# Kernel optimization log

Hardware: AMD Instinct MI355X
Metric: run time of the kernel (lower is better)

Reference implementation:

```python
import jax, jax.numpy as jnp
import numpy as np


def _entropy(x):
    # x: [..., C]; rowwise entropy of softmax(x) along last axis
    logp = jax.nn.log_softmax(x, axis=-1)
    return -(jnp.exp(logp) * logp).sum(-1)


def setup_inputs() -> dict:
    key = jax.random.key(0)
    C, E = 8192, 512
    prototypes = jax.random.normal(key, (C, E), dtype=jnp.float32)
    return {"prototypes": prototypes}


def reference(prototypes):
    C, E = prototypes.shape
    # F.normalize(p=2, dim=1): divide by L2 norm clamped to 1e-12
    norm = jnp.sqrt(jnp.sum(prototypes * prototypes, axis=1, keepdims=True))
    p = prototypes / jnp.maximum(norm, 1e-12)
    # Gram matrix [C, C] (fused matmul instead of broadcast-mul-sum)
    proto_logits = jnp.einsum("ce,de->cd", p, p)
    proto_logits_sum = proto_logits.sum(0, keepdims=True)  # [1, C]
    loss = _entropy(proto_logits).sum(-1) / C + _entropy(proto_logits_sum)
    return loss.sum()
```

## Files before the change

kernel.cpp:

```cpp
#include <hip/hip_runtime.h>
#include <hip/hip_bf16.h>

#define C_DIM 8192
#define E_DIM 512

using f32x4 = __attribute__((ext_vector_type(4))) float;
using i32x4 = __attribute__((ext_vector_type(4))) int;

__device__ inline void gload_lds16(const void* g, void* l) {
  __builtin_amdgcn_global_load_lds(
      (const __attribute__((address_space(1))) unsigned*)g,
      (__attribute__((address_space(3))) unsigned*)l, 16, 0, 0);
}

__device__ inline unsigned pack_bf16(float a, float b) {
  unsigned ua = __float_as_uint(a), ub = __float_as_uint(b);
  ua = (ua + 0x7fffu + ((ua >> 16) & 1u)) >> 16;
  ub = (ub + 0x7fffu + ((ub >> 16) & 1u)) >> 16;
  return ua | (ub << 16);
}

__device__ inline float bf2f(unsigned short u) {
  return __uint_as_float(((unsigned)u) << 16);
}

__device__ inline unsigned pack_i8x4(float a, float b, float c, float d) {
  unsigned x0 = (unsigned)(__float2int_rn(a * 127.f)) & 255u;
  unsigned x1 = (unsigned)(__float2int_rn(b * 127.f)) & 255u;
  unsigned x2 = (unsigned)(__float2int_rn(c * 127.f)) & 255u;
  unsigned x3 = (unsigned)(__float2int_rn(d * 127.f)) & 255u;
  return x0 | (x1 << 8) | (x2 << 16) | (x3 << 24);
}

__global__ __launch_bounds__(256) void norm_kernel(
    const float* __restrict__ P, unsigned* __restrict__ Pb,
    unsigned* __restrict__ Pi) {
  int wid = threadIdx.x >> 6, lane = threadIdx.x & 63;
  int row = blockIdx.x * 4 + wid;
  const float4* src = (const float4*)(P + (size_t)row * E_DIM);
  float4 v0 = src[lane], v1 = src[lane + 64];
  float ss = v0.x * v0.x + v0.y * v0.y + v0.z * v0.z + v0.w * v0.w +
             v1.x * v1.x + v1.y * v1.y + v1.z * v1.z + v1.w * v1.w;
  for (int m = 32; m; m >>= 1) ss += __shfl_xor(ss, m);
  float inv = 1.0f / fmaxf(sqrtf(ss), 1e-12f);
  v0.x *= inv; v0.y *= inv; v0.z *= inv; v0.w *= inv;
  v1.x *= inv; v1.y *= inv; v1.z *= inv; v1.w *= inv;
  uint2* bd = (uint2*)(Pb + (size_t)row * (E_DIM / 2));
  uint2 b0, b1;
  b0.x = pack_bf16(v0.x, v0.y); b0.y = pack_bf16(v0.z, v0.w);
  b1.x = pack_bf16(v1.x, v1.y); b1.y = pack_bf16(v1.z, v1.w);
  bd[lane] = b0; bd[lane + 64] = b1;
  Pi[(size_t)row * 128 + lane] = pack_i8x4(v0.x, v0.y, v0.z, v0.w);
  Pi[(size_t)row * 128 + 64 + lane] = pack_i8x4(v1.x, v1.y, v1.z, v1.w);
}

__global__ __launch_bounds__(256) void qsum_kernel(
    const unsigned short* __restrict__ Pb, float* __restrict__ q) {
  __shared__ float red[4][512];
  int wid = threadIdx.x >> 6, lane = threadIdx.x & 63;
  float a[8];
#pragma unroll
  for (int k = 0; k < 8; ++k) a[k] = 0.f;
  for (int i = 0; i < 32; ++i) {
    int row = blockIdx.x * 128 + wid * 32 + i;
    uint4 v = *(const uint4*)(Pb + (size_t)row * E_DIM + lane * 8);
    a[0] += bf2f((unsigned short)(v.x & 0xffff));
    a[1] += bf2f((unsigned short)(v.x >> 16));
    a[2] += bf2f((unsigned short)(v.y & 0xffff));
    a[3] += bf2f((unsigned short)(v.y >> 16));
    a[4] += bf2f((unsigned short)(v.z & 0xffff));
    a[5] += bf2f((unsigned short)(v.z >> 16));
    a[6] += bf2f((unsigned short)(v.w & 0xffff));
    a[7] += bf2f((unsigned short)(v.w >> 16));
  }
#pragma unroll
  for (int k = 0; k < 8; ++k) red[wid][lane * 8 + k] = a[k];
  __syncthreads();
  for (int c = threadIdx.x; c < 512; c += 256) {
    float t = red[0][c] + red[1][c] + red[2][c] + red[3][c];
    atomicAdd(&q[c], t);
  }
}

__global__ __launch_bounds__(256) void ssum_kernel(
    const unsigned short* __restrict__ Pb, const float* __restrict__ q,
    float* __restrict__ s) {
  int wid = threadIdx.x >> 6, lane = threadIdx.x & 63;
  int row = blockIdx.x * 4 + wid;
  uint4 v = *(const uint4*)(Pb + (size_t)row * E_DIM + lane * 8);
  const float4* qv = (const float4*)q;
  float4 q0 = qv[lane * 2], q1 = qv[lane * 2 + 1];
  float d = bf2f((unsigned short)(v.x & 0xffff)) * q0.x +
            bf2f((unsigned short)(v.x >> 16)) * q0.y +
            bf2f((unsigned short)(v.y & 0xffff)) * q0.z +
            bf2f((unsigned short)(v.y >> 16)) * q0.w +
            bf2f((unsigned short)(v.z & 0xffff)) * q1.x +
            bf2f((unsigned short)(v.z >> 16)) * q1.y +
            bf2f((unsigned short)(v.w & 0xffff)) * q1.z +
            bf2f((unsigned short)(v.w >> 16)) * q1.w;
  for (int m = 32; m; m >>= 1) d += __shfl_xor(d, m);
  if (lane == 0) s[row] = d;
}

__global__ __launch_bounds__(256) void gram_kernel(
    const unsigned char* __restrict__ Pi, float* __restrict__ Zp,
    float* __restrict__ Sp) {
  __shared__ unsigned char As[128 * 128];
  __shared__ unsigned char Bs[128 * 128];

  int b = blockIdx.x;
  int i = (b & 7) * 260 + (b >> 3);
  float bi = 64.5f - sqrtf(64.5f * 64.5f - 2.0f * (float)i);
  int by = (int)bi;
  if (by < 0) by = 0;
  while (64 * (by + 1) - ((by + 1) * by) / 2 <= i) ++by;
  while (64 * by - (by * (by - 1)) / 2 > i) --by;
  int bx = by + (i - (64 * by - (by * (by - 1)) / 2));
  bool diag = (bx == by);

  int tid = threadIdx.x, wid = tid >> 6, lane = tid & 63;
  int wr = wid >> 1, wc = wid & 1;
  int l15 = lane & 15, lh = lane >> 4;

  i32x4 acc[4][4];
#pragma unroll
  for (int m = 0; m < 4; ++m)
#pragma unroll
    for (int n = 0; n < 4; ++n)
      acc[m][n] = (i32x4){0, 0, 0, 0};

  int rs = lane >> 3;
  int gsw = (lane & 7) ^ rs;
  const unsigned char* abase = Pi + (size_t)(by * 128) * E_DIM;
  const unsigned char* bbase = Pi + (size_t)(bx * 128) * E_DIM;

  for (int kt = 0; kt < 4; ++kt) {
#pragma unroll
    for (int j = 0; j < 4; ++j) {
      int ci = wid * 4 + j;
      int r = ci * 8 + rs;
      gload_lds16(abase + (size_t)r * E_DIM + kt * 128 + gsw * 16,
                  (char*)As + ci * 1024);
      gload_lds16(bbase + (size_t)r * E_DIM + kt * 128 + gsw * 16,
                  (char*)Bs + ci * 1024);
    }
    __syncthreads();

    i32x4 af[4][2], bfr[4][2];
#pragma unroll
    for (int m = 0; m < 4; ++m)
#pragma unroll
      for (int kk = 0; kk < 2; ++kk) {
        int row = wr * 64 + m * 16 + l15;
        int g = (kk * 4 + lh) ^ (row & 7);
        af[m][kk] = *(const i32x4*)(As + row * 128 + g * 16);
      }
#pragma unroll
    for (int n = 0; n < 4; ++n)
#pragma unroll
      for (int kk = 0; kk < 2; ++kk) {
        int row = wc * 64 + n * 16 + l15;
        int g = (kk * 4 + lh) ^ (row & 7);
        bfr[n][kk] = *(const i32x4*)(Bs + row * 128 + g * 16);
      }

#pragma unroll
    for (int kk = 0; kk < 2; ++kk)
#pragma unroll
      for (int m = 0; m < 4; ++m)
#pragma unroll
        for (int n = 0; n < 4; ++n)
          acc[m][n] = __builtin_amdgcn_mfma_i32_16x16x64_i8(
              af[m][kk], bfr[n][kk], acc[m][n], 0, 0, 0);
    if (kt < 3) __syncthreads();
  }

  const float invq = 1.0f / 16129.0f;
  float zc[4], sc[4];
#pragma unroll
  for (int n = 0; n < 4; ++n) { zc[n] = 0.f; sc[n] = 0.f; }

  int slotR = bx * 2 + wc;
#pragma unroll
  for (int m = 0; m < 4; ++m) {
#pragma unroll
    for (int reg = 0; reg < 4; ++reg) {
      float z = 0.f, s = 0.f;
#pragma unroll
      for (int n = 0; n < 4; ++n) {
        float g = (float)acc[m][n][reg] * invq;
        float e = __expf(g);
        z += e;
        s += e * g;
        zc[n] += e;
        sc[n] += e * g;
      }
      for (int msk = 8; msk; msk >>= 1) {
        z += __shfl_xor(z, msk);
        s += __shfl_xor(s, msk);
      }
      if (l15 == 0) {
        int rowin = wr * 64 + m * 16 + lh * 4 + reg;
        size_t idx = (size_t)by * 16384 + (size_t)slotR * 128 + rowin;
        Zp[idx] = z;
        Sp[idx] = s;
      }
    }
  }
  if (!diag) {
    int slotC = by * 2 + wr;
#pragma unroll
    for (int n = 0; n < 4; ++n) {
      float z = zc[n], s = sc[n];
      z += __shfl_xor(z, 16); s += __shfl_xor(s, 16);
      z += __shfl_xor(z, 32); s += __shfl_xor(s, 32);
      if (lh == 0) {
        int colin = wc * 64 + n * 16 + l15;
        size_t idx = (size_t)bx * 16384 + (size_t)slotC * 128 + colin;
        Zp[idx] = z;
        Sp[idx] = s;
      }
    }
  }
}

__global__ __launch_bounds__(256) void reduce_kernel(
    const float* __restrict__ Zp, const float* __restrict__ Sp,
    float* __restrict__ Hrow) {
  __shared__ float zbuf[128], sbuf[128];
  int rb = blockIdx.x;
  int t = threadIdx.x;
  int row = t & 127;
  const float* src = (t >= 128) ? Sp : Zp;
  size_t base = (size_t)rb * 16384 + row;
  float acc = 0.f;
#pragma unroll 8
  for (int sl = 0; sl < 128; ++sl) acc += src[base + (size_t)sl * 128];
  if (t >= 128) sbuf[row] = acc; else zbuf[row] = acc;
  __syncthreads();
  if (t < 128) {
    float z = zbuf[t], s2 = sbuf[t];
    Hrow[rb * 128 + t] = logf(z) - s2 / z;
  }
}

__device__ inline float bsum(float v, volatile float* red) {
  int lane = threadIdx.x & 63, wid = threadIdx.x >> 6;
  for (int k = 32; k; k >>= 1) v += __shfl_xor(v, k);
  __syncthreads();
  if (lane == 0) red[wid] = v;
  __syncthreads();
  float r = 0.f;
  if (wid == 0) {
    r = (lane < 16) ? red[lane] : 0.f;
    for (int k = 8; k; k >>= 1) r += __shfl_xor(r, k);
  }
  if (threadIdx.x == 0) red[16] = r;
  __syncthreads();
  return red[16];
}

__device__ inline float bmax(float v, volatile float* red) {
  int lane = threadIdx.x & 63, wid = threadIdx.x >> 6;
  for (int k = 32; k; k >>= 1) v = fmaxf(v, __shfl_xor(v, k));
  __syncthreads();
  if (lane == 0) red[wid] = v;
  __syncthreads();
  float r = -3.4e38f;
  if (wid == 0) {
    r = (lane < 16) ? red[lane] : -3.4e38f;
    for (int k = 8; k; k >>= 1) r = fmaxf(r, __shfl_xor(r, k));
  }
  if (threadIdx.x == 0) red[16] = r;
  __syncthreads();
  return red[16];
}

__global__ __launch_bounds__(1024) void final_kernel(
    const float* __restrict__ s, const float* __restrict__ Hrow,
    float* __restrict__ out) {
  __shared__ float red[17];
  int tid = threadIdx.x;

  float m = -3.4e38f;
  for (int i = tid; i < C_DIM; i += 1024) m = fmaxf(m, s[i]);
  m = bmax(m, red);

  float z = 0.f, sw = 0.f;
  for (int i = tid; i < C_DIM; i += 1024) {
    float t = s[i] - m;
    float e = __expf(t);
    z += e;
    sw += e * t;
  }
  z = bsum(z, red);
  sw = bsum(sw, red);
  float H2 = logf(z) - sw / z;

  float h = 0.f;
  for (int i = tid; i < C_DIM; i += 1024) h += Hrow[i];
  h = bsum(h, red);

  if (tid == 0) out[0] = h / (float)C_DIM + H2;
}

extern "C" void kernel_launch(void* const* d_in, const int* in_sizes, int n_in,
                              void* d_out, int out_size, void* d_ws, size_t ws_size,
                              hipStream_t stream) {
  const float* P = (const float*)d_in[0];
  float* out = (float*)d_out;

  char* ws = (char*)d_ws;
  unsigned* Pb = (unsigned*)ws;
  unsigned* Pi = (unsigned*)(ws + ((size_t)8 << 20));
  float* Zp = (float*)(ws + ((size_t)12 << 20));
  float* Sp = (float*)(ws + ((size_t)16 << 20));
  float* q = (float*)(ws + ((size_t)20 << 20));
  float* s = (float*)(ws + ((size_t)20 << 20) + 4096);
  float* Hrow = (float*)(ws + ((size_t)20 << 20) + 4096 + 32768);

  hipMemsetAsync(q, 0, 2048, stream);

  norm_kernel<<<C_DIM / 4, 256, 0, stream>>>(P, Pb, Pi);
  qsum_kernel<<<C_DIM / 128, 256, 0, stream>>>((const unsigned short*)Pb, q);
  ssum_kernel<<<C_DIM / 4, 256, 0, stream>>>((const unsigned short*)Pb, q, s);
  gram_kernel<<<2080, 256, 0, stream>>>((const unsigned char*)Pi, Zp, Sp);
  reduce_kernel<<<64, 256, 0, stream>>>(Zp, Sp, Hrow);
  final_kernel<<<1, 1024, 0, stream>>>(s, Hrow, out);
}
```

Baseline: 82.55 us.

## Enlarge gram tiles to 256x256 with 16-wave blocks and MFMA priority

The int8 Gram kernel now computes 256x256 output tiles per block with 16 waves (1024 threads) instead of 128x128 with 4 waves, cutting the triangular grid from 2080 to 528 blocks and halving global loads per output element. The k-loop is restructured to load fragments per kk step, which lowers register pressure, and MFMA sections are wrapped in s_setprio. Partial Z/S slot indexing is remapped so the existing 128-row reduce layout still works. The risks are fewer blocks for load balance across CUs, larger LDS per block, and launch_bounds(1024,4) limiting registers.

```diff
diff --git a/kernel.cpp b/kernel.cpp
--- a/kernel.cpp
+++ b/kernel.cpp
@@ -102,24 +102,24 @@
   if (lane == 0) s[row] = d;
 }
 
-__global__ __launch_bounds__(256) void gram_kernel(
+__global__ __launch_bounds__(1024, 4) void gram_kernel(
     const unsigned char* __restrict__ Pi, float* __restrict__ Zp,
     float* __restrict__ Sp) {
-  __shared__ unsigned char As[128 * 128];
-  __shared__ unsigned char Bs[128 * 128];
+  __shared__ unsigned char As[256 * 128];
+  __shared__ unsigned char Bs[256 * 128];
 
   int b = blockIdx.x;
-  int i = (b & 7) * 260 + (b >> 3);
-  float bi = 64.5f - sqrtf(64.5f * 64.5f - 2.0f * (float)i);
+  int i = (b & 7) * 66 + (b >> 3);
+  float bi = 32.5f - sqrtf(32.5f * 32.5f - 2.0f * (float)i);
   int by = (int)bi;
   if (by < 0) by = 0;
-  while (64 * (by + 1) - ((by + 1) * by) / 2 <= i) ++by;
-  while (64 * by - (by * (by - 1)) / 2 > i) --by;
-  int bx = by + (i - (64 * by - (by * (by - 1)) / 2));
+  while (32 * (by + 1) - ((by + 1) * by) / 2 <= i) ++by;
+  while (32 * by - (by * (by - 1)) / 2 > i) --by;
+  int bx = by + (i - (32 * by - (by * (by - 1)) / 2));
   bool diag = (bx == by);
 
   int tid = threadIdx.x, wid = tid >> 6, lane = tid & 63;
-  int wr = wid >> 1, wc = wid & 1;
+  int wr = wid >> 2, wc = wid & 3;
   int l15 = lane & 15, lh = lane >> 4;
 
   i32x4 acc[4][4];
@@ -131,13 +131,14 @@
 
   int rs = lane >> 3;
   int gsw = (lane & 7) ^ rs;
-  const unsigned char* abase = Pi + (size_t)(by * 128) * E_DIM;
-  const unsigned char* bbase = Pi + (size_t)(bx * 128) * E_DIM;
+  const unsigned char* abase = Pi + (size_t)(by * 256) * E_DIM;
+  const unsigned char* bbase = Pi + (size_t)(bx * 256) * E_DIM;
 
   for (int kt = 0; kt < 4; ++kt) {
-#pragma unroll
-    for (int j = 0; j < 4; ++j) {
-      int ci = wid * 4 + j;
+    if (kt > 0) __syncthreads();
+#pragma unroll
+    for (int j = 0; j < 2; ++j) {
+      int ci = wid * 2 + j;
       int r = ci * 8 + rs;
       gload_lds16(abase + (size_t)r * E_DIM + kt * 128 + gsw * 16,
                   (char*)As + ci * 1024);
@@ -146,33 +147,30 @@
     }
     __syncthreads();
 
-    i32x4 af[4][2], bfr[4][2];
-#pragma unroll
-    for (int m = 0; m < 4; ++m)
-#pragma unroll
-      for (int kk = 0; kk < 2; ++kk) {
+#pragma unroll
+    for (int kk = 0; kk < 2; ++kk) {
+      i32x4 af[4], bfr[4];
+#pragma unroll
+      for (int m = 0; m < 4; ++m) {
         int row = wr * 64 + m * 16 + l15;
         int g = (kk * 4 + lh) ^ (row & 7);
-        af[m][kk] = *(const i32x4*)(As + row * 128 + g * 16);
-      }
-#pragma unroll
-    for (int n = 0; n < 4; ++n)
-#pragma unroll
-      for (int kk = 0; kk < 2; ++kk) {
+        af[m] = *(const i32x4*)(As + row * 128 + g * 16);
+      }
+#pragma unroll
+      for (int n = 0; n < 4; ++n) {
         int row = wc * 64 + n * 16 + l15;
         int g = (kk * 4 + lh) ^ (row & 7);
-        bfr[n][kk] = *(const i32x4*)(Bs + row * 128 + g * 16);
-      }
-
-#pragma unroll
-    for (int kk = 0; kk < 2; ++kk)
+        bfr[n] = *(const i32x4*)(Bs + row * 128 + g * 16);
+      }
+      __builtin_amdgcn_s_setprio(1);
 #pragma unroll
       for (int m = 0; m < 4; ++m)
 #pragma unroll
         for (int n = 0; n < 4; ++n)
           acc[m][n] = __builtin_amdgcn_mfma_i32_16x16x64_i8(
-              af[m][kk], bfr[n][kk], acc[m][n], 0, 0, 0);
-    if (kt < 3) __syncthreads();
+              af[m], bfr[n], acc[m][n], 0, 0, 0);
+      __builtin_amdgcn_s_setprio(0);
+    }
   }
 
   const float invq = 1.0f / 16129.0f;
@@ -180,7 +178,8 @@
 #pragma unroll
   for (int n = 0; n < 4; ++n) { zc[n] = 0.f; sc[n] = 0.f; }
 
-  int slotR = bx * 2 + wc;
+  int bandR = 2 * by + (wr >> 1);
+  int cslotR = (bx - by) * 4 + wc;
 #pragma unroll
   for (int m = 0; m < 4; ++m) {
 #pragma unroll
@@ -200,23 +199,24 @@
         s += __shfl_xor(s, msk);
       }
       if (l15 == 0) {
-        int rowin = wr * 64 + m * 16 + lh * 4 + reg;
-        size_t idx = (size_t)by * 16384 + (size_t)slotR * 128 + rowin;
+        int rowin = (wr & 1) * 64 + m * 16 + lh * 4 + reg;
+        size_t idx = (size_t)bandR * 16384 + (size_t)cslotR * 128 + rowin;
         Zp[idx] = z;
         Sp[idx] = s;
       }
     }
   }
   if (!diag) {
-    int slotC = by * 2 + wr;
+    int bandC = 2 * bx + (wc >> 1);
+    int cslotC = 128 - 4 * bx + by * 4 + wr;
 #pragma unroll
     for (int n = 0; n < 4; ++n) {
       float z = zc[n], s = sc[n];
       z += __shfl_xor(z, 16); s += __shfl_xor(s, 16);
       z += __shfl_xor(z, 32); s += __shfl_xor(s, 32);
       if (lh == 0) {
-        int colin = wc * 64 + n * 16 + l15;
-        size_t idx = (size_t)bx * 16384 + (size_t)slotC * 128 + colin;
+        int colin = (wc & 1) * 64 + n * 16 + l15;
+        size_t idx = (size_t)bandC * 16384 + (size_t)cslotC * 128 + colin;
         Zp[idx] = z;
         Sp[idx] = s;
       }
@@ -324,7 +324,7 @@
   norm_kernel<<<C_DIM / 4, 256, 0, stream>>>(P, Pb, Pi);
   qsum_kernel<<<C_DIM / 128, 256, 0, stream>>>((const unsigned short*)Pb, q);
   ssum_kernel<<<C_DIM / 4, 256, 0, stream>>>((const unsigned short*)Pb, q, s);
-  gram_kernel<<<2080, 256, 0, stream>>>((const unsigned char*)Pi, Zp, Sp);
+  gram_kernel<<<528, 1024, 0, stream>>>((const unsigned char*)Pi, Zp, Sp);
   reduce_kernel<<<64, 256, 0, stream>>>(Zp, Sp, Hrow);
   final_kernel<<<1, 1024, 0, stream>>>(s, Hrow, out);
 }
```

Result: slower. 91.47 us (+10.8%).
